# Performance work log

Measured on AMD Instinct MI355X. Metric: run time of the kernel, lower is better.

Reference implementation:

```python
import jax, jax.numpy as jnp
import numpy as np

THRESHOLD = 0.5
NEG_POS = 3
ALPHA = 1.0


def cxcy_to_xy(c):
    return jnp.concatenate([c[..., :2] - c[..., 2:] / 2, c[..., :2] + c[..., 2:] / 2], axis=-1)


def xy_to_cxcy(x):
    return jnp.concatenate([(x[..., :2] + x[..., 2:]) / 2, x[..., 2:] - x[..., :2]], axis=-1)


def encode_gcxgcy(cxcy, priors_cxcy):
    # SSD offset encoding with variances (10, 10, 5, 5)
    return jnp.concatenate([
        (cxcy[..., :2] - priors_cxcy[..., :2]) / (priors_cxcy[..., 2:] / 10.0),
        jnp.log(cxcy[..., 2:] / priors_cxcy[..., 2:]) * 5.0,
    ], axis=-1)


def compute_iou(a, b):
    # a: [n,4] xyxy, b: [m,4] xyxy -> [n,m]
    lt = jnp.maximum(a[:, None, :2], b[None, :, :2])
    rb = jnp.minimum(a[:, None, 2:], b[None, :, 2:])
    wh = jnp.clip(rb - lt, 0.0)
    inter = wh[..., 0] * wh[..., 1]
    area_a = (a[:, 2] - a[:, 0]) * (a[:, 3] - a[:, 1])
    area_b = (b[:, 2] - b[:, 0]) * (b[:, 3] - b[:, 1])
    return inter / (area_a[:, None] + area_b[None, :] - inter)


def _match_one(boxes, labels, db_xy, db_cxcy):
    # boxes: [n_obj,4] xyxy, labels: [n_obj], priors: [P,4]
    n_obj = boxes.shape[0]
    overlaps = compute_iou(boxes, db_xy)                 # [n_obj, P]
    ov_per_box = jnp.max(overlaps, axis=0)               # [P]
    obj_per_box = jnp.argmax(overlaps, axis=0)           # [P]
    box_per_obj = jnp.argmax(overlaps, axis=1)           # [n_obj]
    # force each gt to own its best prior
    obj_per_box = obj_per_box.at[box_per_obj].set(jnp.arange(n_obj))
    ov_per_box = ov_per_box.at[box_per_obj].set(1.0)
    lbl = labels[obj_per_box]                            # [P]
    lbl = jnp.where(ov_per_box < THRESHOLD, 0, lbl)      # background below threshold
    true_locs = encode_gcxgcy(xy_to_cxcy(boxes[obj_per_box]), db_cxcy)  # [P,4]
    return true_locs, lbl


def smooth_l1(x):
    ax = jnp.abs(x)
    return jnp.where(ax < 1.0, 0.5 * x * x, ax - 0.5)


def reference(loc_pred, cls_pred, gt_boxes, gt_labels, default_boxes):
    # loc_pred: [B,P,4], cls_pred: [B,P,C], gt_boxes: [B,n_obj,4],
    # gt_labels: [B,n_obj] int, default_boxes: [P,4] cxcywh
    db_xy = cxcy_to_xy(default_boxes)
    true_locs, true_labels = jax.vmap(_match_one, in_axes=(0, 0, None, None))(
        gt_boxes, gt_labels, db_xy, default_boxes)      # [B,P,4], [B,P]

    positive = true_labels > 0                           # [B,P]
    n_pos = jnp.sum(positive, axis=1)                    # [B]
    n_pos_total = jnp.sum(n_pos).astype(loc_pred.dtype)

    # localization loss: SmoothL1 mean over positive box elements
    loc_elem = smooth_l1(loc_pred - true_locs)           # [B,P,4]
    loc_loss = jnp.sum(loc_elem * positive[..., None]) / (n_pos_total * 4.0)

    # confidence loss: cross entropy with 3:1 hard negative mining
    logp = jax.nn.log_softmax(cls_pred, axis=-1)         # [B,P,C]
    ce = -jnp.take_along_axis(logp, true_labels[..., None], axis=-1)[..., 0]  # [B,P]
    conf_pos = jnp.sum(ce * positive)
    ce_neg = jnp.where(positive, 0.0, ce)
    # rank negatives by loss (descending) per image; take top neg_pos * n_pos
    ranks = jnp.argsort(jnp.argsort(-ce_neg, axis=1), axis=1)  # [B,P]
    hard_neg = ranks < (NEG_POS * n_pos)[:, None]
    conf_hard = jnp.sum(ce_neg * hard_neg)
    conf_loss = (conf_pos + conf_hard) / n_pos_total

    return conf_loss + ALPHA * loc_loss


def setup_inputs() -> dict:
    key = jax.random.key(0)
    ks = jax.random.split(key, 8)
    B, P, C, n_obj = 64, 8732, 81, 32

    # priors in cxcywh, valid in [0,1]
    db_cxy = jax.random.uniform(ks[0], (P, 2), minval=0.05, maxval=0.95)
    db_wh = jax.random.uniform(ks[1], (P, 2), minval=0.05, maxval=0.3)
    default_boxes = jnp.concatenate([db_cxy, db_wh], axis=-1).astype(jnp.float32)

    # gt boxes: valid xyxy built from centers and sizes
    g_cxy = jax.random.uniform(ks[2], (B, n_obj, 2), minval=0.2, maxval=0.8)
    g_wh = jax.random.uniform(ks[3], (B, n_obj, 2), minval=0.1, maxval=0.4)
    gt_boxes = jnp.concatenate([g_cxy - g_wh / 2, g_cxy + g_wh / 2], axis=-1).astype(jnp.float32)
    gt_labels = jax.random.randint(ks[4], (B, n_obj), 1, C)

    loc_pred = jax.random.normal(ks[5], (B, P, 4), dtype=jnp.float32) * 0.1
    cls_pred = jax.random.normal(ks[6], (B, P, C), dtype=jnp.float32)

    return {"loc_pred": loc_pred, "cls_pred": cls_pred, "gt_boxes": gt_boxes,
            "gt_labels": gt_labels, "default_boxes": default_boxes}
```

## Files before the change

kernel.cpp:

```cpp
#include <hip/hip_runtime.h>
#include <hip/hip_bf16.h>
#include <math.h>

#define BB 64
#define PP 8732
#define CC 81
#define NOBJ 32
#define CHUNKS ((PP + 255) / 256)
#define NPRI (BB * PP)
#define WTILE 16
#define WTW (WTILE * CC)
#define NWT (NPRI / WTILE)
#define CE_BLOCKS 2048

typedef float f4 __attribute__((ext_vector_type(4)));

__device__ __forceinline__ float sl1(float x) {
    float ax = fabsf(x);
    return (ax < 1.0f) ? 0.5f * x * x : ax - 0.5f;
}

__global__ __launch_bounds__(256) void k_ce(
    const float* __restrict__ cls_pred,
    float* __restrict__ lse,
    float* __restrict__ ce_neg)
{
    const int tid  = threadIdx.x;
    const int wave = tid >> 6, lane = tid & 63;
    const int rloc = lane >> 2, q = lane & 3;
    const int NW   = CE_BLOCKS * 4;

    const int seg_start = rloc * CC + q * 20;
    const int seg_len   = (q == 3) ? 21 : 20;
    const int ws        = seg_start >> 2;
    const int a         = seg_start & 3;
    const int hi_cnt    = a + seg_len - 20;

    const float L2E = 1.4426950408889634f;
    const float LN2 = 0.6931471805599453f;

    for (int wt = blockIdx.x * 4 + wave; wt < NWT; wt += NW) {
        const f4* src = reinterpret_cast<const f4*>(cls_pred) + (size_t)wt * (WTW / 4) + ws;
        f4 w0 = src[0];
        f4 w1 = src[1];
        f4 w2 = src[2];
        f4 w3 = src[3];
        f4 w4 = src[4];
        f4 w5 = src[5];

        float s0 = 0.0f, s1 = 0.0f;
#pragma unroll
        for (int k = 0; k < 4; ++k) {
            float e = exp2f(w0[k] * L2E);
            s0 += (k >= a) ? e : 0.0f;
        }
#pragma unroll
        for (int k = 0; k < 4; ++k) s1 += exp2f(w1[k] * L2E);
#pragma unroll
        for (int k = 0; k < 4; ++k) s0 += exp2f(w2[k] * L2E);
#pragma unroll
        for (int k = 0; k < 4; ++k) s1 += exp2f(w3[k] * L2E);
#pragma unroll
        for (int k = 0; k < 4; ++k) s0 += exp2f(w4[k] * L2E);
#pragma unroll
        for (int k = 0; k < 4; ++k) {
            float e = exp2f(w5[k] * L2E);
            s1 += (k < hi_cnt) ? e : 0.0f;
        }
        float s = s0 + s1;
        s += __shfl_xor(s, 1);
        s += __shfl_xor(s, 2);

        if (q == 0) {
            float x0 = w0[a];
            float l  = log2f(s) * LN2;
            const int pidx = wt * WTILE + rloc;
            lse[pidx]    = l;
            ce_neg[pidx] = fmaxf(l - x0, 0.0f);
        }
    }
}

__global__ __launch_bounds__(256) void k_bestprior(
    const float* __restrict__ gt_boxes,
    const float* __restrict__ dbox,
    int*   __restrict__ bp,
    float* __restrict__ acc,
    int*   __restrict__ npt,
    int*   __restrict__ done,
    int*   __restrict__ n_pos)
{
    __shared__ float s_bv[4];
    __shared__ int   s_bi[4];
    const int tid = threadIdx.x, lane = tid & 63, wave = tid >> 6;
    const int b = blockIdx.x >> 5;
    const int o = blockIdx.x & 31;

    if (blockIdx.x == 0) {
        if (tid < BB) n_pos[tid] = 0;
        else if (tid < BB + 3) acc[tid - BB] = 0.0f;
        else if (tid == BB + 3) *npt = 0;
        else if (tid == BB + 4) *done = 0;
    }

    const float* g = gt_boxes + (b * NOBJ + o) * 4;
    float gx0 = g[0], gy0 = g[1], gx1 = g[2], gy1 = g[3];
    float garea = (gx1 - gx0) * (gy1 - gy0);

    float best = -1.0f; int bpp = 0x7fffffff;
    for (int p = tid; p < PP; p += 256) {
        float4 db = reinterpret_cast<const float4*>(dbox)[p];
        float px0 = db.x - db.z * 0.5f, py0 = db.y - db.w * 0.5f;
        float px1 = db.x + db.z * 0.5f, py1 = db.y + db.w * 0.5f;
        float parea = db.z * db.w;
        float lx = fmaxf(px0, gx0), ly = fmaxf(py0, gy0);
        float rx = fminf(px1, gx1), ry = fminf(py1, gy1);
        float w = fmaxf(rx - lx, 0.0f), h = fmaxf(ry - ly, 0.0f);
        float inter = w * h;
        float iou = inter / (garea + parea - inter);
        if (iou > best) { best = iou; bpp = p; }
    }
#pragma unroll
    for (int m = 32; m > 0; m >>= 1) {
        float ov = __shfl_xor(best, m);
        int   op = __shfl_xor(bpp, m);
        if (ov > best || (ov == best && op < bpp)) { best = ov; bpp = op; }
    }
    if (lane == 0) { s_bv[wave] = best; s_bi[wave] = bpp; }
    __syncthreads();
    if (tid == 0) {
        for (int w2 = 1; w2 < 4; ++w2) {
            if (s_bv[w2] > best || (s_bv[w2] == best && s_bi[w2] < bpp)) {
                best = s_bv[w2]; bpp = s_bi[w2];
            }
        }
        bp[b * NOBJ + o] = bpp;
    }
}

__global__ __launch_bounds__(256) void k_assign(
    const float* __restrict__ loc_pred,
    const float* __restrict__ gt_boxes,
    const int*   __restrict__ gt_labels,
    const float* __restrict__ dbox,
    const int*   __restrict__ bp,
    const float* __restrict__ cls_pred,
    const float* __restrict__ lse,
    float* __restrict__ ce_neg,
    int*   __restrict__ n_pos,
    float* __restrict__ acc,
    int*   __restrict__ n_pos_total)
{
    __shared__ float s_gx0[NOBJ], s_gy0[NOBJ], s_gx1[NOBJ], s_gy1[NOBJ], s_garea[NOBJ];
    __shared__ float s_gcx[NOBJ], s_gcy[NOBJ], s_gw[NOBJ], s_gh[NOBJ];
    __shared__ int   s_glbl[NOBJ], s_bp[NOBJ];
    __shared__ float red_f[256], red_g[256];
    __shared__ int   red_i[256];

    const int b     = blockIdx.x / CHUNKS;
    const int chunk = blockIdx.x % CHUNKS;
    const int tid   = threadIdx.x;
    const int p     = chunk * 256 + tid;

    if (tid < NOBJ) {
        float x0 = gt_boxes[(b * NOBJ + tid) * 4 + 0];
        float y0 = gt_boxes[(b * NOBJ + tid) * 4 + 1];
        float x1 = gt_boxes[(b * NOBJ + tid) * 4 + 2];
        float y1 = gt_boxes[(b * NOBJ + tid) * 4 + 3];
        s_gx0[tid] = x0; s_gy0[tid] = y0; s_gx1[tid] = x1; s_gy1[tid] = y1;
        s_garea[tid] = (x1 - x0) * (y1 - y0);
        s_gcx[tid] = (x0 + x1) * 0.5f;
        s_gcy[tid] = (y0 + y1) * 0.5f;
        s_gw[tid]  = x1 - x0;
        s_gh[tid]  = y1 - y0;
        s_glbl[tid] = gt_labels[b * NOBJ + tid];
        s_bp[tid]   = bp[b * NOBJ + tid];
    }
    __syncthreads();

    float loc_local = 0.0f, pos_local = 0.0f;
    int   np_local  = 0;

    if (p < PP) {
        const int idx = b * PP + p;
        float4 db = reinterpret_cast<const float4*>(dbox)[p];
        float px0 = db.x - db.z * 0.5f, py0 = db.y - db.w * 0.5f;
        float px1 = db.x + db.z * 0.5f, py1 = db.y + db.w * 0.5f;
        float parea = db.z * db.w;

        float best = -1.0f; int bo = 0;
#pragma unroll
        for (int o = 0; o < NOBJ; ++o) {
            float lx = fmaxf(px0, s_gx0[o]), ly = fmaxf(py0, s_gy0[o]);
            float rx = fminf(px1, s_gx1[o]), ry = fminf(py1, s_gy1[o]);
            float w = fmaxf(rx - lx, 0.0f), h = fmaxf(ry - ly, 0.0f);
            float inter = w * h;
            float iou = inter / (s_garea[o] + parea - inter);
            if (iou > best) { best = iou; bo = o; }
        }
        int forced = -1;
#pragma unroll
        for (int o = 0; o < NOBJ; ++o)
            if (s_bp[o] == p) forced = o;

        int o_use, lbl;
        if (forced >= 0) { o_use = forced; lbl = s_glbl[forced]; }
        else             { o_use = bo; lbl = (best < 0.5f) ? 0 : s_glbl[bo]; }

        if (lbl > 0) {
            np_local = 1;
            ce_neg[idx] = 0.0f;
            float xl = cls_pred[(size_t)idx * CC + lbl];
            pos_local = fmaxf(lse[idx] - xl, 0.0f);
            float g0 = (s_gcx[o_use] - db.x) / (db.z / 10.0f);
            float g1 = (s_gcy[o_use] - db.y) / (db.w / 10.0f);
            float g2 = logf(s_gw[o_use] / db.z) * 5.0f;
            float g3 = logf(s_gh[o_use] / db.w) * 5.0f;
            float4 lp = reinterpret_cast<const float4*>(loc_pred)[idx];
            loc_local = sl1(lp.x - g0) + sl1(lp.y - g1) + sl1(lp.z - g2) + sl1(lp.w - g3);
        }
    }

    red_f[tid] = loc_local;
    red_g[tid] = pos_local;
    red_i[tid] = np_local;
    __syncthreads();
#pragma unroll
    for (int st = 128; st > 0; st >>= 1) {
        if (tid < st) {
            red_f[tid] += red_f[tid + st];
            red_g[tid] += red_g[tid + st];
            red_i[tid] += red_i[tid + st];
        }
        __syncthreads();
    }
    if (tid == 0) {
        if (red_f[0] != 0.0f) atomicAdd(&acc[0], red_f[0]);
        if (red_g[0] != 0.0f) atomicAdd(&acc[1], red_g[0]);
        if (red_i[0]) {
            atomicAdd(&n_pos[b], red_i[0]);
            atomicAdd(n_pos_total, red_i[0]);
        }
    }
}

__global__ __launch_bounds__(1024) void k_select(
    const float* __restrict__ ce_neg,
    const int*   __restrict__ n_pos,
    float* __restrict__ acc,
    const int*  __restrict__ n_pos_total,
    int*   __restrict__ done,
    float* __restrict__ out)
{
    __shared__ unsigned int sv[PP];
    __shared__ unsigned int h16[16][256];
    __shared__ unsigned int hist[257];
    __shared__ unsigned int wtot[4];
    __shared__ unsigned int s_prefix, s_krem;
    __shared__ float rf[16];
    __shared__ int   ri[16];

    const int b = blockIdx.x, tid = threadIdx.x;
    const int lane = tid & 63, w = tid >> 6;

    int K = n_pos[b] * 3;
    if (K > PP) K = PP;

    if (K > 0) {
        for (int i = tid; i < PP; i += 1024)
            sv[i] = __float_as_uint(ce_neg[b * PP + i]);

        unsigned int prefix = 0, krem = (unsigned int)K;
        for (int shift = 24; shift >= 0; shift -= 8) {
            unsigned int* hflat = &h16[0][0];
            for (int j = tid; j < 16 * 256; j += 1024) hflat[j] = 0;
            if (tid == 0) hist[256] = 0;
            __syncthreads();
            unsigned int mask_hi = (shift == 24) ? 0u : (0xFFFFFFFFu << (shift + 8));
            for (int i = tid; i < PP; i += 1024) {
                unsigned int v = sv[i];
                if ((v & mask_hi) == prefix)
                    atomicAdd(&h16[w][(v >> shift) & 0xFFu], 1u);
            }
            __syncthreads();
            unsigned int s = 0;
            if (tid < 256) {
#pragma unroll
                for (int r = 0; r < 16; ++r) s += h16[r][tid];
#pragma unroll
                for (int off = 1; off < 64; off <<= 1) {
                    unsigned int a = __shfl_down(s, off);
                    if (lane + off < 64) s += a;
                }
                if (lane == 0) wtot[w] = s;
            }
            __syncthreads();
            if (tid < 256) {
                unsigned int sb = 0;
#pragma unroll
                for (int r = 0; r < 16; ++r) sb += h16[r][tid];
                unsigned int suf = sb;
#pragma unroll
                for (int off = 1; off < 64; off <<= 1) {
                    unsigned int a = __shfl_down(suf, off);
                    if (lane + off < 64) suf += a;
                }
                for (int w2 = w + 1; w2 < 4; ++w2) suf += wtot[w2];
                hist[tid] = suf;
            }
            __syncthreads();
            if (tid < 256) {
                unsigned int suf  = hist[tid];
                unsigned int suf1 = hist[tid + 1];
                if (suf >= krem && suf1 < krem) {
                    s_prefix = prefix | ((unsigned int)tid << shift);
                    s_krem   = krem - suf1;
                }
            }
            __syncthreads();
            prefix = s_prefix; krem = s_krem;
        }
        float cutoff = __uint_as_float(prefix);

        float sum_gt = 0.0f; int cnt_gt = 0;
        for (int i = tid; i < PP; i += 1024) {
            float v = __uint_as_float(sv[i]);
            if (v > cutoff) { sum_gt += v; cnt_gt++; }
        }
#pragma unroll
        for (int m = 32; m > 0; m >>= 1) {
            sum_gt += __shfl_xor(sum_gt, m);
            cnt_gt += __shfl_xor(cnt_gt, m);
        }
        if (lane == 0) { rf[w] = sum_gt; ri[w] = cnt_gt; }
        __syncthreads();
        if (tid == 0) {
            float sg = 0.0f; int cg = 0;
#pragma unroll
            for (int r = 0; r < 16; ++r) { sg += rf[r]; cg += ri[r]; }
            atomicAdd(&acc[2], sg + (float)(K - cg) * cutoff);
        }
    }

    if (tid == 0) {
        __threadfence();
        int old = atomicAdd(done, 1);
        if (old == BB - 1) {
            float a0 = atomicAdd(&acc[0], 0.0f);
            float a1 = atomicAdd(&acc[1], 0.0f);
            float a2 = atomicAdd(&acc[2], 0.0f);
            float npt = (float)atomicAdd((int*)n_pos_total, 0);
            out[0] = (a1 + a2) / npt + a0 / (npt * 4.0f);
        }
    }
}

extern "C" void kernel_launch(void* const* d_in, const int* in_sizes, int n_in,
                              void* d_out, int out_size, void* d_ws, size_t ws_size,
                              hipStream_t stream) {
    const float* loc_pred  = (const float*)d_in[0];
    const float* cls_pred  = (const float*)d_in[1];
    const float* gt_boxes  = (const float*)d_in[2];
    const int*   gt_labels = (const int*)d_in[3];
    const float* dbox      = (const float*)d_in[4];
    float* out = (float*)d_out;

    float* acc    = (float*)d_ws;
    int*   npt    = (int*)d_ws + 3;
    int*   done   = (int*)d_ws + 4;
    int*   n_pos  = (int*)d_ws + 8;
    int*   bp     = (int*)d_ws + 8 + BB;
    float* lse    = (float*)((int*)d_ws + 8 + BB + BB * NOBJ);
    float* ce_neg = lse + (size_t)NPRI;

    k_ce<<<CE_BLOCKS, 256, 0, stream>>>(cls_pred, lse, ce_neg);
    k_bestprior<<<BB * NOBJ, 256, 0, stream>>>(gt_boxes, dbox, bp,
                                               acc, npt, done, n_pos);
    k_assign<<<BB * CHUNKS, 256, 0, stream>>>(loc_pred, gt_boxes, gt_labels, dbox, bp,
                                              cls_pred, lse, ce_neg, n_pos, acc, npt);
    k_select<<<BB, 1024, 0, stream>>>(ce_neg, n_pos, acc, npt, done, out);
}
```

Baseline: 164.9 us.

## Fuse best-prior search into assign kernel and stage CE tiles through LDS with prefetch

Removes the separate best-prior kernel. Each k_match block now computes every ground-truth box's best prior itself, with 8 lanes per object, before assigning a quarter of the priors. The counter initialisation moves into k_ce. k_ce now loads each tile with coalesced nontemporal loads into LDS and prefetches the next tile in registers, and the CE grid drops to 1792 blocks. This saves one launch and improves load coalescing, at the cost of redoing the best-prior scan four times per image and running k_match with only 256 blocks.

```diff
diff --git a/kernel.cpp b/kernel.cpp
--- a/kernel.cpp
+++ b/kernel.cpp
@@ -6,12 +6,12 @@
 #define PP 8732
 #define CC 81
 #define NOBJ 32
-#define CHUNKS ((PP + 255) / 256)
 #define NPRI (BB * PP)
 #define WTILE 16
 #define WTW (WTILE * CC)
 #define NWT (NPRI / WTILE)
-#define CE_BLOCKS 2048
+#define CE_BLOCKS 1792
+#define QP (PP / 4)
 
 typedef float f4 __attribute__((ext_vector_type(4)));
 
@@ -23,12 +23,28 @@
 __global__ __launch_bounds__(256) void k_ce(
     const float* __restrict__ cls_pred,
     float* __restrict__ lse,
-    float* __restrict__ ce_neg)
+    float* __restrict__ ce_neg,
+    float* __restrict__ acc,
+    int*   __restrict__ npt,
+    int*   __restrict__ done,
+    int*   __restrict__ n_pos)
 {
+    __shared__ float s_x[4][WTW];
     const int tid  = threadIdx.x;
     const int wave = tid >> 6, lane = tid & 63;
     const int rloc = lane >> 2, q = lane & 3;
     const int NW   = CE_BLOCKS * 4;
+
+    if (blockIdx.x == 0) {
+        if (tid < BB) n_pos[tid] = 0;
+        else if (tid < BB + 3) acc[tid - BB] = 0.0f;
+        else if (tid == BB + 3) *npt = 0;
+        else if (tid == BB + 4) *done = 0;
+    }
+
+    float* sx = s_x[wave];
+    f4* dst = reinterpret_cast<f4*>(sx);
+    const f4* tile4 = reinterpret_cast<const f4*>(sx);
 
     const int seg_start = rloc * CC + q * 20;
     const int seg_len   = (q == 3) ? 21 : 20;
@@ -39,14 +55,41 @@
     const float L2E = 1.4426950408889634f;
     const float LN2 = 0.6931471805599453f;
 
-    for (int wt = blockIdx.x * 4 + wave; wt < NWT; wt += NW) {
-        const f4* src = reinterpret_cast<const f4*>(cls_pred) + (size_t)wt * (WTW / 4) + ws;
-        f4 w0 = src[0];
-        f4 w1 = src[1];
-        f4 w2 = src[2];
-        f4 w3 = src[3];
-        f4 w4 = src[4];
-        f4 w5 = src[5];
+    int wt = blockIdx.x * 4 + wave;
+    f4 r0, r1, r2, r3, r4, r5;
+    if (wt < NWT) {
+        const f4* src = reinterpret_cast<const f4*>(cls_pred + (size_t)wt * WTW);
+        r0 = __builtin_nontemporal_load(src + lane);
+        r1 = __builtin_nontemporal_load(src + 64 + lane);
+        r2 = __builtin_nontemporal_load(src + 128 + lane);
+        r3 = __builtin_nontemporal_load(src + 192 + lane);
+        r4 = __builtin_nontemporal_load(src + 256 + lane);
+        if (lane < 4) r5 = __builtin_nontemporal_load(src + 320 + lane);
+    }
+
+    while (wt < NWT) {
+        dst[lane] = r0; dst[64 + lane] = r1; dst[128 + lane] = r2;
+        dst[192 + lane] = r3; dst[256 + lane] = r4;
+        if (lane < 4) dst[320 + lane] = r5;
+        const int pidx = wt * WTILE + rloc;
+
+        wt += NW;
+        if (wt < NWT) {
+            const f4* src = reinterpret_cast<const f4*>(cls_pred + (size_t)wt * WTW);
+            r0 = __builtin_nontemporal_load(src + lane);
+            r1 = __builtin_nontemporal_load(src + 64 + lane);
+            r2 = __builtin_nontemporal_load(src + 128 + lane);
+            r3 = __builtin_nontemporal_load(src + 192 + lane);
+            r4 = __builtin_nontemporal_load(src + 256 + lane);
+            if (lane < 4) r5 = __builtin_nontemporal_load(src + 320 + lane);
+        }
+
+        f4 w0 = tile4[ws];
+        f4 w1 = tile4[ws + 1];
+        f4 w2 = tile4[ws + 2];
+        f4 w3 = tile4[ws + 3];
+        f4 w4 = tile4[ws + 4];
+        f4 w5 = tile4[ws + 5];
 
         float s0 = 0.0f, s1 = 0.0f;
 #pragma unroll
@@ -72,78 +115,19 @@
         s += __shfl_xor(s, 2);
 
         if (q == 0) {
-            float x0 = w0[a];
             float l  = log2f(s) * LN2;
-            const int pidx = wt * WTILE + rloc;
+            float x0 = sx[rloc * CC];
             lse[pidx]    = l;
             ce_neg[pidx] = fmaxf(l - x0, 0.0f);
         }
     }
 }
 
-__global__ __launch_bounds__(256) void k_bestprior(
-    const float* __restrict__ gt_boxes,
-    const float* __restrict__ dbox,
-    int*   __restrict__ bp,
-    float* __restrict__ acc,
-    int*   __restrict__ npt,
-    int*   __restrict__ done,
-    int*   __restrict__ n_pos)
-{
-    __shared__ float s_bv[4];
-    __shared__ int   s_bi[4];
-    const int tid = threadIdx.x, lane = tid & 63, wave = tid >> 6;
-    const int b = blockIdx.x >> 5;
-    const int o = blockIdx.x & 31;
-
-    if (blockIdx.x == 0) {
-        if (tid < BB) n_pos[tid] = 0;
-        else if (tid < BB + 3) acc[tid - BB] = 0.0f;
-        else if (tid == BB + 3) *npt = 0;
-        else if (tid == BB + 4) *done = 0;
-    }
-
-    const float* g = gt_boxes + (b * NOBJ + o) * 4;
-    float gx0 = g[0], gy0 = g[1], gx1 = g[2], gy1 = g[3];
-    float garea = (gx1 - gx0) * (gy1 - gy0);
-
-    float best = -1.0f; int bpp = 0x7fffffff;
-    for (int p = tid; p < PP; p += 256) {
-        float4 db = reinterpret_cast<const float4*>(dbox)[p];
-        float px0 = db.x - db.z * 0.5f, py0 = db.y - db.w * 0.5f;
-        float px1 = db.x + db.z * 0.5f, py1 = db.y + db.w * 0.5f;
-        float parea = db.z * db.w;
-        float lx = fmaxf(px0, gx0), ly = fmaxf(py0, gy0);
-        float rx = fminf(px1, gx1), ry = fminf(py1, gy1);
-        float w = fmaxf(rx - lx, 0.0f), h = fmaxf(ry - ly, 0.0f);
-        float inter = w * h;
-        float iou = inter / (garea + parea - inter);
-        if (iou > best) { best = iou; bpp = p; }
-    }
-#pragma unroll
-    for (int m = 32; m > 0; m >>= 1) {
-        float ov = __shfl_xor(best, m);
-        int   op = __shfl_xor(bpp, m);
-        if (ov > best || (ov == best && op < bpp)) { best = ov; bpp = op; }
-    }
-    if (lane == 0) { s_bv[wave] = best; s_bi[wave] = bpp; }
-    __syncthreads();
-    if (tid == 0) {
-        for (int w2 = 1; w2 < 4; ++w2) {
-            if (s_bv[w2] > best || (s_bv[w2] == best && s_bi[w2] < bpp)) {
-                best = s_bv[w2]; bpp = s_bi[w2];
-            }
-        }
-        bp[b * NOBJ + o] = bpp;
-    }
-}
-
-__global__ __launch_bounds__(256) void k_assign(
+__global__ __launch_bounds__(256) void k_match(
     const float* __restrict__ loc_pred,
     const float* __restrict__ gt_boxes,
     const int*   __restrict__ gt_labels,
     const float* __restrict__ dbox,
-    const int*   __restrict__ bp,
     const float* __restrict__ cls_pred,
     const float* __restrict__ lse,
     float* __restrict__ ce_neg,
@@ -157,10 +141,10 @@
     __shared__ float red_f[256], red_g[256];
     __shared__ int   red_i[256];
 
-    const int b     = blockIdx.x / CHUNKS;
-    const int chunk = blockIdx.x % CHUNKS;
-    const int tid   = threadIdx.x;
-    const int p     = chunk * 256 + tid;
+    const int tid  = threadIdx.x;
+    const int wave = tid >> 6, lane = tid & 63;
+    const int b       = blockIdx.x >> 2;
+    const int quarter = blockIdx.x & 3;
 
     if (tid < NOBJ) {
         float x0 = gt_boxes[(b * NOBJ + tid) * 4 + 0];
@@ -174,14 +158,42 @@
         s_gw[tid]  = x1 - x0;
         s_gh[tid]  = y1 - y0;
         s_glbl[tid] = gt_labels[b * NOBJ + tid];
-        s_bp[tid]   = bp[b * NOBJ + tid];
+    }
+    __syncthreads();
+
+    {
+        const int o = wave * 8 + (lane >> 3);
+        const float gx0 = s_gx0[o], gy0 = s_gy0[o], gx1 = s_gx1[o], gy1 = s_gy1[o];
+        const float garea = s_garea[o];
+
+        float best = -1.0f; int bpp = 0x7fffffff;
+        for (int p = (lane & 7); p < PP; p += 8) {
+            float4 db = reinterpret_cast<const float4*>(dbox)[p];
+            float px0 = db.x - db.z * 0.5f, py0 = db.y - db.w * 0.5f;
+            float px1 = db.x + db.z * 0.5f, py1 = db.y + db.w * 0.5f;
+            float parea = db.z * db.w;
+            float lx = fmaxf(px0, gx0), ly = fmaxf(py0, gy0);
+            float rx = fminf(px1, gx1), ry = fminf(py1, gy1);
+            float w = fmaxf(rx - lx, 0.0f), h = fmaxf(ry - ly, 0.0f);
+            float inter = w * h;
+            float iou = inter / (garea + parea - inter);
+            if (iou > best) { best = iou; bpp = p; }
+        }
+#pragma unroll
+        for (int m = 1; m < 8; m <<= 1) {
+            float ov = __shfl_xor(best, m);
+            int   op = __shfl_xor(bpp, m);
+            if (ov > best || (ov == best && op < bpp)) { best = ov; bpp = op; }
+        }
+        if ((lane & 7) == 0) s_bp[o] = bpp;
     }
     __syncthreads();
 
     float loc_local = 0.0f, pos_local = 0.0f;
     int   np_local  = 0;
 
-    if (p < PP) {
+    for (int i = tid; i < QP; i += 256) {
+        const int p   = quarter * QP + i;
         const int idx = b * PP + p;
         float4 db = reinterpret_cast<const float4*>(dbox)[p];
         float px0 = db.x - db.z * 0.5f, py0 = db.y - db.w * 0.5f;
@@ -208,16 +220,17 @@
         else             { o_use = bo; lbl = (best < 0.5f) ? 0 : s_glbl[bo]; }
 
         if (lbl > 0) {
-            np_local = 1;
+            np_local++;
             ce_neg[idx] = 0.0f;
             float xl = cls_pred[(size_t)idx * CC + lbl];
-            pos_local = fmaxf(lse[idx] - xl, 0.0f);
+            pos_local += fmaxf(lse[idx] - xl, 0.0f);
             float g0 = (s_gcx[o_use] - db.x) / (db.z / 10.0f);
             float g1 = (s_gcy[o_use] - db.y) / (db.w / 10.0f);
             float g2 = logf(s_gw[o_use] / db.z) * 5.0f;
             float g3 = logf(s_gh[o_use] / db.w) * 5.0f;
             float4 lp = reinterpret_cast<const float4*>(loc_pred)[idx];
-            loc_local = sl1(lp.x - g0) + sl1(lp.y - g1) + sl1(lp.z - g2) + sl1(lp.w - g3);
+            loc_local += sl1(lp.x - g0) + sl1(lp.y - g1)
+                       + sl1(lp.z - g2) + sl1(lp.w - g3);
         }
     }
 
@@ -289,8 +302,8 @@
                 for (int r = 0; r < 16; ++r) s += h16[r][tid];
 #pragma unroll
                 for (int off = 1; off < 64; off <<= 1) {
-                    unsigned int a = __shfl_down(s, off);
-                    if (lane + off < 64) s += a;
+                    unsigned int aa = __shfl_down(s, off);
+                    if (lane + off < 64) s += aa;
                 }
                 if (lane == 0) wtot[w] = s;
             }
@@ -302,8 +315,8 @@
                 unsigned int suf = sb;
 #pragma unroll
                 for (int off = 1; off < 64; off <<= 1) {
-                    unsigned int a = __shfl_down(suf, off);
-                    if (lane + off < 64) suf += a;
+                    unsigned int aa = __shfl_down(suf, off);
+                    if (lane + off < 64) suf += aa;
                 }
                 for (int w2 = w + 1; w2 < 4; ++w2) suf += wtot[w2];
                 hist[tid] = suf;
@@ -369,14 +382,12 @@
     int*   npt    = (int*)d_ws + 3;
     int*   done   = (int*)d_ws + 4;
     int*   n_pos  = (int*)d_ws + 8;
-    int*   bp     = (int*)d_ws + 8 + BB;
-    float* lse    = (float*)((int*)d_ws + 8 + BB + BB * NOBJ);
+    float* lse    = (float*)((int*)d_ws + 8 + BB);
     float* ce_neg = lse + (size_t)NPRI;
 
-    k_ce<<<CE_BLOCKS, 256, 0, stream>>>(cls_pred, lse, ce_neg);
-    k_bestprior<<<BB * NOBJ, 256, 0, stream>>>(gt_boxes, dbox, bp,
-                                               acc, npt, done, n_pos);
-    k_assign<<<BB * CHUNKS, 256, 0, stream>>>(loc_pred, gt_boxes, gt_labels, dbox, bp,
-                                              cls_pred, lse, ce_neg, n_pos, acc, npt);
+    k_ce<<<CE_BLOCKS, 256, 0, stream>>>(cls_pred, lse, ce_neg,
+                                        acc, npt, done, n_pos);
+    k_match<<<BB * 4, 256, 0, stream>>>(loc_pred, gt_boxes, gt_labels, dbox,
+                                        cls_pred, lse, ce_neg, n_pos, acc, npt);
     k_select<<<BB, 1024, 0, stream>>>(ce_neg, n_pos, acc, npt, done, out);
 }
```

After: 350.1 us. 112% more time.
